# Performance work log

Measured on AMD Instinct MI355X. Metric: run time of the kernel, lower is better.

## Reference

```python
import jax, jax.numpy as jnp
import numpy as np

N = 25000
E = 400000
MUL0 = 64   # multiplicity of 0e node irreps
MUL1 = 32   # multiplicity of 1o node irreps
NUM_BASIS = 10
FC_HIDDEN = 100
WEIGHT_NUMEL = 2 * MUL0 + 3 * MUL1  # 224: per-edge tp weights for the 5 uvu paths
MID_S = MUL0 + MUL1       # 96 mid scalar channels
MID_V = MUL0 + 2 * MUL1   # 128 mid vector channels
NUM_NEIGHBORS = 16.0


def setup_inputs() -> dict:
    key = jax.random.key(0)
    ks = jax.random.split(key, 16)
    inp = {
        'node_scalars': jax.random.normal(ks[0], (N, MUL0), jnp.float32),
        'node_vectors': jax.random.normal(ks[1], (N, MUL1, 3), jnp.float32),
        'node_attr': jnp.ones((N, 1), jnp.float32),
        'edge_src': jax.random.randint(ks[2], (E,), 0, N, jnp.int32),
        'edge_dst': jax.random.randint(ks[3], (E,), 0, N, jnp.int32),
        'edge_attr': jax.random.normal(ks[4], (E, 4), jnp.float32),
        'edge_scalars': jax.random.normal(ks[5], (E, NUM_BASIS), jnp.float32),
        # FullyConnectedNet: [10, 100, weight_numel], silu on hidden
        'W_fc1': jax.random.normal(ks[6], (NUM_BASIS, FC_HIDDEN), jnp.float32) / np.sqrt(NUM_BASIS),
        'W_fc2': jax.random.normal(ks[7], (FC_HIDDEN, WEIGHT_NUMEL), jnp.float32) / np.sqrt(FC_HIDDEN),
        # FullyConnectedTensorProduct with 0e attr == per-irrep linear mixing
        'W_sc_s': jax.random.normal(ks[8], (MUL0, MUL0), jnp.float32) / np.sqrt(MUL0),
        'W_sc_v': jax.random.normal(ks[9], (MUL1, MUL1), jnp.float32) / np.sqrt(MUL1),
        'W_l1_s': jax.random.normal(ks[10], (MUL0, MUL0), jnp.float32) / np.sqrt(MUL0),
        'W_l1_v': jax.random.normal(ks[11], (MUL1, MUL1), jnp.float32) / np.sqrt(MUL1),
        'W_l2_s': jax.random.normal(ks[12], (MID_S, MUL0), jnp.float32) / np.sqrt(MID_S),
        'W_l2_v': jax.random.normal(ks[13], (MID_V, MUL1), jnp.float32) / np.sqrt(MID_V),
        'W_l3': jax.random.normal(ks[14], (MID_S, 1), jnp.float32) / np.sqrt(MID_S),
    }
    return inp


def reference(node_scalars, node_vectors, node_attr, edge_src, edge_dst, edge_attr,
              edge_scalars, W_fc1, W_fc2, W_sc_s, W_sc_v, W_l1_s, W_l1_v,
              W_l2_s, W_l2_v, W_l3):
    n = node_scalars.shape[0]
    # --- edge-weight FC net: silu hidden, linear out -> per-edge tp weights ---
    w = jax.nn.silu(edge_scalars @ W_fc1) @ W_fc2  # [E, 224]
    w_00, w_01 = w[:, :MUL0], w[:, MUL0:2 * MUL0]                  # paths from 0e input
    w_10 = w[:, 2 * MUL0:2 * MUL0 + MUL1]                          # 1o x 0e -> 1o
    w_11s = w[:, 2 * MUL0 + MUL1:2 * MUL0 + 2 * MUL1]              # 1o x 1o -> 0e
    w_11v = w[:, 2 * MUL0 + 2 * MUL1:]                             # 1o x 1o -> 1o

    attr = node_attr  # [N,1] (0e attr => scalar multiplier)
    # self-connection and lin1 (per-irrep linear * attr)
    sc_s = (node_scalars @ W_sc_s) * attr
    sc_v = jnp.einsum('nuc,uv->nvc', node_vectors, W_sc_v) * attr[:, :, None]
    f_s = (node_scalars @ W_l1_s) * attr
    f_v = jnp.einsum('nuc,uv->nvc', node_vectors, W_l1_v) * attr[:, :, None]

    # --- gather source node features per edge ---
    s = f_s[edge_src]          # [E, MUL0]
    v = f_v[edge_src]          # [E, MUL1, 3]
    y0 = edge_attr[:, :1]      # l=0 sh
    y1 = edge_attr[:, 1:4]     # l=1 sh

    # --- weighted tensor product (uvu), CG-contracted paths ---
    mid_s = jnp.concatenate([
        w_00 * s * y0,                                              # 0e x 0e -> 0e
        w_11s * jnp.einsum('euc,ec->eu', v, y1) / jnp.sqrt(3.0),    # 1o x 1o -> 0e
    ], axis=1)                                                      # [E, 96]
    mid_v = jnp.concatenate([
        w_01[:, :, None] * s[:, :, None] * y1[:, None, :],          # 0e x 1o -> 1o
        w_10[:, :, None] * v * y0[:, :, None],                      # 1o x 0e -> 1o
        w_11v[:, :, None] * jnp.cross(v, y1[:, None, :]) / jnp.sqrt(2.0),  # 1o x 1o -> 1o
    ], axis=1)                                                      # [E, 128, 3]

    # --- scatter-add aggregation into destination nodes ---
    inv = 1.0 / jnp.sqrt(NUM_NEIGHBORS)
    agg_s = jax.ops.segment_sum(mid_s, edge_dst, num_segments=n) * inv
    agg_v = jax.ops.segment_sum(mid_v, edge_dst, num_segments=n) * inv

    # --- output linears and gated residual mix ---
    conv_s = (agg_s @ W_l2_s) * attr
    conv_v = jnp.einsum('nuc,uv->nvc', agg_v, W_l2_v) * attr[:, :, None]
    angle = 0.1 * (agg_s @ W_l3) * attr  # [N,1]
    cos, sin = jnp.cos(angle), jnp.sin(angle)  # sc output_mask is all-ones here
    out_s = cos * sc_s + sin * conv_s
    out_v = cos[:, :, None] * sc_v + sin[:, :, None] * conv_v
    return jnp.concatenate([out_s, out_v.reshape(n, -1)], axis=1)  # [N, 64+96]
```

## Files before the change

### kernel.cpp

```cpp
#include <hip/hip_runtime.h>

#define MUL0 64
#define MUL1 32
#define NBASIS 10
#define FCH 100
#define WNUMEL 224
#define MIDS 96
#define MIDV 128
#define EG 4

#define OFF_W1   0
#define OFF_W2   1000
#define OFF_WSCS 23400
#define OFF_WSCV 27496
#define OFF_WL1S 28520
#define OFF_WL1V 32616
#define OFF_WL2S 33640
#define OFF_WL2V 39784
#define OFF_WL3  43880
#define OFF_WEND 43976
#define OFF_FLAG 43980
#define OFF_W1FRAG 44032
#define OFF_W2FRAG 45824
#define OFF_DYN  60160

#define W1FRAG_N (112 * 32)
#define W2FRAG_N (4 * 224 * 32)

typedef __attribute__((ext_vector_type(8))) short short8;
typedef __attribute__((ext_vector_type(4))) float f32x4;

__device__ __forceinline__ float bf2f(unsigned short h) {
    unsigned int u = ((unsigned int)h) << 16;
    float f; __builtin_memcpy(&f, &u, 4); return f;
}
__device__ __forceinline__ unsigned short f2bf(float f) {
    unsigned int u; __builtin_memcpy(&u, &f, 4);
    u += 0x7fffu + ((u >> 16) & 1u);
    return (unsigned short)(u >> 16);
}
__device__ __forceinline__ float fast_silu(float x) {
    return x * __builtin_amdgcn_rcpf(1.0f + __expf(-x));
}
template<bool BF>
__device__ __forceinline__ float ldf(const void* p, size_t i) {
    if constexpr (BF) return bf2f(((const unsigned short*)p)[i]);
    else              return ((const float*)p)[i];
}
template<bool BF>
__device__ __forceinline__ void stf(void* p, size_t i, float v) {
    if constexpr (BF) ((unsigned short*)p)[i] = f2bf(v);
    else              ((float*)p)[i] = v;
}
template<bool BF>
__device__ __forceinline__ f32x4 ld4(const void* p, size_t i) {
    if constexpr (BF) {
        ushort4 h = *(const ushort4*)((const unsigned short*)p + i);
        return (f32x4){bf2f(h.x), bf2f(h.y), bf2f(h.z), bf2f(h.w)};
    } else {
        return *(const f32x4*)((const float*)p + i);
    }
}
__device__ __forceinline__ int wave_incl_scan(int v) {
    int lane = threadIdx.x & 63;
    #pragma unroll
    for (int d = 1; d < 64; d <<= 1) {
        int t = __shfl_up(v, d, 64);
        if (lane >= d) v += t;
    }
    return v;
}

template<bool BF>
__device__ __forceinline__ void node_pre_body(
    const void* __restrict__ ns, const void* __restrict__ nv,
    const void* __restrict__ attr,
    const void* __restrict__ Wl1s, const void* __restrict__ Wl1v,
    float* __restrict__ f_s, float* __restrict__ f_v, int i, int Nn)
{
    int stotal = Nn * MUL0;
    if (i < stotal) {
        int n = i >> 6, j = i & 63;
        float a = 0.f;
        #pragma unroll
        for (int u = 0; u < MUL0; u++)
            a = fmaf(ldf<BF>(ns, (size_t)n * MUL0 + u), ldf<BF>(Wl1s, u * MUL0 + j), a);
        f_s[i] = a * ldf<BF>(attr, n);
    } else {
        int m = i - stotal;
        if (m >= Nn * MUL1 * 3) return;
        int n = m / 96; int idx = m - n * 96;
        int vi = idx / 3; int c = idx - vi * 3;
        float a = 0.f;
        #pragma unroll
        for (int u = 0; u < MUL1; u++)
            a = fmaf(ldf<BF>(nv, (size_t)n * 96 + u * 3 + c), ldf<BF>(Wl1v, u * MUL1 + vi), a);
        f_v[m] = a * ldf<BF>(attr, n);
    }
}

__global__ __launch_bounds__(256) void k_prep(
    const void* __restrict__ ns, const void* __restrict__ nv,
    const void* __restrict__ attr,
    const void* __restrict__ a0, const void* __restrict__ a1,
    const void* __restrict__ a2, const void* __restrict__ a3,
    const void* __restrict__ a4, const void* __restrict__ a5,
    const void* __restrict__ a6, const void* __restrict__ a7,
    const void* __restrict__ a8,
    float* __restrict__ wsf,
    unsigned short* __restrict__ w1frag, unsigned short* __restrict__ w2frag,
    int* __restrict__ cnt, int* __restrict__ flag,
    float* __restrict__ f_s, float* __restrict__ f_v, int Nn)
{
    const bool bf = (((const unsigned int*)attr)[0] == 0x3F803F80u);
    int i = blockIdx.x * 256 + threadIdx.x;
    if (i == 0) *flag = bf ? 1 : 0;

    const int npre = Nn * 160;
    if (i < npre) {
        if (bf) node_pre_body<true >(ns, nv, attr, a4, a5, f_s, f_v, i, Nn);
        else    node_pre_body<false>(ns, nv, attr, a4, a5, f_s, f_v, i, Nn);
        return;
    }
    int m = i - npre;
    if (m < OFF_WEND) {
        const void* p; int off = m;
        if      (m < OFF_W2)   { p = a0; }
        else if (m < OFF_WSCS) { p = a1; off = m - OFF_W2; }
        else if (m < OFF_WSCV) { p = a2; off = m - OFF_WSCS; }
        else if (m < OFF_WL1S) { p = a3; off = m - OFF_WSCV; }
        else if (m < OFF_WL1V) { p = a4; off = m - OFF_WL1S; }
        else if (m < OFF_WL2S) { p = a5; off = m - OFF_WL1V; }
        else if (m < OFF_WL2V) { p = a6; off = m - OFF_WL2S; }
        else if (m < OFF_WL3)  { p = a7; off = m - OFF_WL2V; }
        else                   { p = a8; off = m - OFF_WL3; }
        wsf[m] = bf ? ldf<true>(p, off) : ldf<false>(p, off);
        return;
    }
    m -= OFF_WEND;
    if (m < W1FRAG_N) {
        int col = m >> 5, k = m & 31;
        float v = 0.f;
        if (col < FCH && k < NBASIS)
            v = bf ? ldf<true>(a0, k * FCH + col) : ldf<false>(a0, k * FCH + col);
        w1frag[m] = f2bf(v);
        return;
    }
    m -= W1FRAG_N;
    if (m < W2FRAG_N) {
        int q = m / (224 * 32); int r = m - q * 224 * 32;
        int n = r >> 5; int kk = r & 31;
        int k = q * 32 + kk;
        float v = 0.f;
        if (k < FCH)
            v = bf ? ldf<true>(a1, k * WNUMEL + n) : ldf<false>(a1, k * WNUMEL + n);
        w2frag[m] = f2bf(v);
        return;
    }
    m -= W2FRAG_N;
    if (m < Nn) cnt[m] = 0;
}

__global__ __launch_bounds__(256) void k_hist(
    const int* __restrict__ edst, int* __restrict__ cnt, int Ecnt)
{
    int e = blockIdx.x * 256 + threadIdx.x;
    if (e < Ecnt) atomicAdd(&cnt[edst[e]], 1);
}

__global__ __launch_bounds__(256) void k_scan_blk(
    const int* __restrict__ cnt, int* __restrict__ row_part,
    int* __restrict__ blk_sum, int Nn)
{
    __shared__ int ws4[4];
    int tid = threadIdx.x, lane = tid & 63, wid = tid >> 6;
    int i = blockIdx.x * 256 + tid;
    int v = (i < Nn) ? cnt[i] : 0;
    int incl = wave_incl_scan(v);
    if (lane == 63) ws4[wid] = incl;
    __syncthreads();
    int off = 0;
    #pragma unroll
    for (int w2 = 0; w2 < 4; w2++) off += (w2 < wid) ? ws4[w2] : 0;
    if (i < Nn) row_part[i] = off + incl - v;
    if (tid == 0) blk_sum[blockIdx.x] = ws4[0] + ws4[1] + ws4[2] + ws4[3];
}

__global__ __launch_bounds__(256) void k_scan_top(
    const int* __restrict__ blk_sum, int* __restrict__ blk_off,
    int* __restrict__ row_start, int NB, int Nn)
{
    __shared__ int ws4[4];
    int tid = threadIdx.x, lane = tid & 63, wid = tid >> 6;
    int v = (tid < NB) ? blk_sum[tid] : 0;
    int incl = wave_incl_scan(v);
    if (lane == 63) ws4[wid] = incl;
    __syncthreads();
    int off = 0;
    #pragma unroll
    for (int w2 = 0; w2 < 4; w2++) off += (w2 < wid) ? ws4[w2] : 0;
    if (tid < NB) blk_off[tid] = off + incl - v;
    if (tid == 0) row_start[Nn] = ws4[0] + ws4[1] + ws4[2] + ws4[3];
}

__global__ __launch_bounds__(256) void k_rowfix(
    const int* __restrict__ row_part, const int* __restrict__ blk_off,
    int* __restrict__ row_start, int* __restrict__ cur, int Nn)
{
    int i = blockIdx.x * 256 + threadIdx.x;
    if (i < Nn) { row_start[i] = blk_off[i >> 8] + row_part[i]; cur[i] = 0; }
}

__global__ __launch_bounds__(1024) void k_scan1(
    const int* __restrict__ cnt, int* __restrict__ row_start,
    int* __restrict__ cur, int Nn)
{
    __shared__ int wsum[16];
    __shared__ int s_off, s_tot;
    int tid = threadIdx.x, lane = tid & 63, wid = tid >> 6;
    if (tid == 0) s_off = 0;
    __syncthreads();
    for (int base = 0; base < Nn; base += 1024) {
        int i = base + tid;
        int v = (i < Nn) ? cnt[i] : 0;
        int incl = wave_incl_scan(v);
        if (lane == 63) wsum[wid] = incl;
        __syncthreads();
        if (wid == 0) {
            int wv = (lane < 16) ? wsum[lane] : 0;
            int wincl = wave_incl_scan(wv);
            if (lane < 16) wsum[lane] = wincl - wv;
            if (lane == 15) s_tot = wincl;
        }
        __syncthreads();
        int excl = s_off + wsum[wid] + incl - v;
        if (i < Nn) { row_start[i] = excl; cur[i] = 0; }
        __syncthreads();
        if (tid == 0) s_off += s_tot;
        __syncthreads();
    }
    if (threadIdx.x == 0) row_start[Nn] = s_off;
}

__global__ __launch_bounds__(256) void k_place(
    const int* __restrict__ edst, const int* __restrict__ esrc,
    const void* __restrict__ eattr,
    const int* __restrict__ row_start, int* __restrict__ cur,
    int* __restrict__ perm, int* __restrict__ srcs, float* __restrict__ y4,
    int Ecnt, const int* __restrict__ flag, int extras)
{
    int e = blockIdx.x * 256 + threadIdx.x;
    if (e >= Ecnt) return;
    int d = edst[e];
    int pos = row_start[d] + atomicAdd(&cur[d], 1);
    perm[pos] = e;
    if (extras) {
        srcs[pos] = esrc[e];
        float4 yv;
        if (*flag) {
            const unsigned short* ap = (const unsigned short*)eattr + (size_t)e * 4;
            yv = make_float4(bf2f(ap[0]), bf2f(ap[1]), bf2f(ap[2]), bf2f(ap[3]));
        } else {
            const float* ap = (const float*)eattr + (size_t)e * 4;
            yv = make_float4(ap[0], ap[1], ap[2], ap[3]);
        }
        ((float4*)y4)[pos] = yv;
    }
}

#define HFC_STRIDE 136

__global__ __launch_bounds__(256) void k_fc(
    const void* __restrict__ escal, const int* __restrict__ perm,
    const unsigned short* __restrict__ w1frag, const unsigned short* __restrict__ w2frag,
    unsigned short* __restrict__ wbuf, int Ecnt, const int* __restrict__ flag)
{
    __shared__ __align__(16) unsigned short h_lds[64 * HFC_STRIDE];
    const int tid  = threadIdx.x;
    const int lane = tid & 63;
    const int wave = tid >> 6;
    const int nl   = lane & 15;
    const int quad = lane >> 4;
    const int tb   = blockIdx.x * 64;

    for (int i = tid; i < 64 * 16; i += 256) {
        int row = i >> 4;
        h_lds[row * HFC_STRIDE + 112 + (i & 15)] = 0;
    }

    int eidx = tb + 16 * wave + nl;
    if (eidx >= Ecnt) eidx = Ecnt - 1;
    const int e = perm[eidx];
    short8 a = {0, 0, 0, 0, 0, 0, 0, 0};
    if (*flag) {
        const unsigned int* p = (const unsigned int*)((const unsigned short*)escal + (size_t)e * NBASIS);
        if (quad == 0) {
            unsigned int d0 = p[0], d1 = p[1], d2 = p[2], d3 = p[3];
            a = (short8){(short)d0, (short)(d0 >> 16), (short)d1, (short)(d1 >> 16),
                         (short)d2, (short)(d2 >> 16), (short)d3, (short)(d3 >> 16)};
        } else if (quad == 1) {
            unsigned int d4 = p[4];
            a = (short8){(short)d4, (short)(d4 >> 16), 0, 0, 0, 0, 0, 0};
        }
    } else {
        const float* p = (const float*)escal + (size_t)e * NBASIS;
        if (quad == 0) {
            a = (short8){(short)f2bf(p[0]), (short)f2bf(p[1]), (short)f2bf(p[2]), (short)f2bf(p[3]),
                         (short)f2bf(p[4]), (short)f2bf(p[5]), (short)f2bf(p[6]), (short)f2bf(p[7])};
        } else if (quad == 1) {
            a = (short8){(short)f2bf(p[8]), (short)f2bf(p[9]), 0, 0, 0, 0, 0, 0};
        }
    }

    {
        f32x4 hacc[7];
        #pragma unroll
        for (int t = 0; t < 7; t++) {
            short8 b = *(const short8*)&w1frag[(16 * t + nl) * 32 + quad * 8];
            hacc[t] = __builtin_amdgcn_mfma_f32_16x16x32_bf16(
                a, b, (f32x4){0.f, 0.f, 0.f, 0.f}, 0, 0, 0);
        }
        #pragma unroll
        for (int t = 0; t < 7; t++) {
            #pragma unroll
            for (int r = 0; r < 4; r++)
                h_lds[(16 * wave + quad * 4 + r) * HFC_STRIDE + 16 * t + nl] =
                    f2bf(fast_silu(hacc[t][r]));
        }
    }
    __syncthreads();

    #pragma unroll 2
    for (int t = 0; t < 14; t++) {
        f32x4 c = {0.f, 0.f, 0.f, 0.f};
        #pragma unroll
        for (int q = 0; q < 4; q++) {
            short8 av = *(const short8*)&h_lds[(16 * wave + nl) * HFC_STRIDE + q * 32 + quad * 8];
            short8 b = *(const short8*)&w2frag[((q * 224) + 16 * t + nl) * 32 + quad * 8];
            c = __builtin_amdgcn_mfma_f32_16x16x32_bf16(av, b, c, 0, 0, 0);
        }
        #pragma unroll
        for (int r = 0; r < 4; r++)
            wbuf[(size_t)(tb + 16 * wave + quad * 4 + r) * WNUMEL + 16 * t + nl] = f2bf(c[r]);
    }
}

__global__ __launch_bounds__(256) void k_agg(
    const unsigned short* __restrict__ wbuf,
    const int* __restrict__ srcs, const float* __restrict__ y4,
    const int* __restrict__ row_start,
    const float* __restrict__ f_s, const float* __restrict__ f_v,
    const float* __restrict__ Wl3, const void* __restrict__ attr,
    float* __restrict__ agg_s, float* __restrict__ aggv,
    float* __restrict__ cosb, float* __restrict__ sinb,
    int Nn, const int* __restrict__ flag)
{
    const int tid  = threadIdx.x;
    const int lane = tid & 63;
    const int wave = tid >> 6;
    const int node = blockIdx.x * EG + wave;
    if (node >= Nn) return;

    const int lane2 = lane & 31;
    const bool hi = (lane >= 32);

    const int dlo = row_start[node];
    const int dhi = row_start[node + 1];

    float acc0 = 0.f, acc1 = 0.f;
    float accS0 = 0.f, accS1 = 0.f, accS2 = 0.f;
    float accV0 = 0.f, accV1 = 0.f, accV2 = 0.f;

    const float k14 = 0.25f;
    const float k13 = 0.25f * 0.57735026918962576451f;
    const float k12 = 0.25f * 0.70710678118654752440f;

    #pragma unroll 2
    for (int idx = dlo; idx < dhi; idx++) {
        const int srcn = srcs[idx];
        const float4 y = ((const float4*)y4)[idx];
        const float y0 = y.x, y1x = y.y, y1y = y.z, y1z = y.w;
        const unsigned short* wrow = wbuf + (size_t)idx * WNUMEL;
        const float* fsr = f_s + (size_t)srcn * 64;
        const float* fvr = f_v + (size_t)srcn * 96;

        float fs_l = fsr[lane];
        float v0 = fvr[lane2 * 3 + 0];
        float v1 = fvr[lane2 * 3 + 1];
        float v2 = fvr[lane2 * 3 + 2];

        float w00 = bf2f(wrow[lane]);
        float w01 = bf2f(wrow[64 + lane]);
        float wh  = bf2f(wrow[128 + lane]);
        float wx  = bf2f(wrow[160 + lane]);

        acc0 = fmaf(w00 * fs_l, y0 * k14, acc0);

        float dot = v0 * y1x + v1 * y1y + v2 * y1z;
        acc1 = fmaf(wh * dot, k13, acc1);

        float t1 = w01 * fs_l * k14;
        accS0 = fmaf(t1, y1x, accS0);
        accS1 = fmaf(t1, y1y, accS1);
        accS2 = fmaf(t1, y1z, accS2);

        float cx = v1 * y1z - v2 * y1y;
        float cy = v2 * y1x - v0 * y1z;
        float cz = v0 * y1y - v1 * y1x;
        float e0 = hi ? cx : v0;
        float e1 = hi ? cy : v1;
        float e2 = hi ? cz : v2;
        float tv = hi ? (wx * k12) : (wh * (y0 * k14));
        accV0 = fmaf(e0, tv, accV0);
        accV1 = fmaf(e1, tv, accV1);
        accV2 = fmaf(e2, tv, accV2);
    }

    {
        float* as = agg_s + (size_t)node * MIDS;
        float* av = aggv  + (size_t)node * 384;
        as[lane] = acc0;
        if (hi) as[64 + lane2] = acc1;

        av[0 * 128 + lane] = accS0;
        av[1 * 128 + lane] = accS1;
        av[2 * 128 + lane] = accS2;
        const int vrow = hi ? (96 + lane2) : (64 + lane);
        av[0 * 128 + vrow] = accV0;
        av[1 * 128 + vrow] = accV1;
        av[2 * 128 + vrow] = accV2;

        float avv = acc0 * Wl3[lane];
        if (hi) avv = fmaf(acc1, Wl3[64 + lane2], avv);
        #pragma unroll
        for (int d = 1; d < 64; d <<= 1) avv += __shfl_xor(avv, d);
        if (lane == 0) {
            float at = (*flag) ? ldf<true>(attr, node) : ldf<false>(attr, node);
            float aa = 0.1f * avv * at;
            cosb[node] = __cosf(aa);
            sinb[node] = __sinf(aa);
        }
    }
}

#define WT_STRIDE 164

template<bool BF>
__device__ __forceinline__ void final_s_body(
    const float* __restrict__ agg_s, const void* __restrict__ ns,
    const float* __restrict__ cosb, const float* __restrict__ sinb,
    const void* __restrict__ attr, void* __restrict__ out,
    int Nn, const float* Wt, int lane, int nb)
{
    float acc_sc[8], acc_l2[8];
    int nidx[8];
    #pragma unroll
    for (int r = 0; r < 8; r++) {
        acc_sc[r] = 0.f; acc_l2[r] = 0.f;
        int n = nb + r; nidx[r] = (n < Nn) ? n : (Nn - 1);
    }
    #pragma unroll 2
    for (int t = 0; t < 16; t++) {
        f32x4 wv = *(const f32x4*)&Wt[lane * WT_STRIDE + 4 * t];
        #pragma unroll
        for (int r = 0; r < 8; r++) {
            f32x4 x = ld4<BF>(ns, (size_t)nidx[r] * 64 + 4 * t);
            acc_sc[r] = fmaf(x[0], wv[0], acc_sc[r]);
            acc_sc[r] = fmaf(x[1], wv[1], acc_sc[r]);
            acc_sc[r] = fmaf(x[2], wv[2], acc_sc[r]);
            acc_sc[r] = fmaf(x[3], wv[3], acc_sc[r]);
        }
    }
    #pragma unroll 2
    for (int t = 0; t < 24; t++) {
        f32x4 wv = *(const f32x4*)&Wt[lane * WT_STRIDE + 64 + 4 * t];
        #pragma unroll
        for (int r = 0; r < 8; r++) {
            f32x4 x = *(const f32x4*)(agg_s + (size_t)nidx[r] * 96 + 4 * t);
            acc_l2[r] = fmaf(x[0], wv[0], acc_l2[r]);
            acc_l2[r] = fmaf(x[1], wv[1], acc_l2[r]);
            acc_l2[r] = fmaf(x[2], wv[2], acc_l2[r]);
            acc_l2[r] = fmaf(x[3], wv[3], acc_l2[r]);
        }
    }
    #pragma unroll
    for (int r = 0; r < 8; r++) {
        int n = nb + r;
        if (n < Nn) {
            float cv = cosb[n], sv = sinb[n];
            float at = ldf<BF>(attr, n);
            stf<BF>(out, (size_t)n * 160 + lane, at * (cv * acc_sc[r] + sv * acc_l2[r]));
        }
    }
}

__global__ __launch_bounds__(256) void k_final_s(
    const float* __restrict__ agg_s, const void* __restrict__ ns,
    const float* __restrict__ Wscs, const float* __restrict__ Wl2s,
    const float* __restrict__ cosb, const float* __restrict__ sinb,
    const void* __restrict__ attr, void* __restrict__ out,
    int Nn, const int* __restrict__ flag)
{
    __shared__ float Wt[64 * WT_STRIDE];
    const int tid = threadIdx.x;
    for (int i = tid; i < 160 * 64; i += 256) {
        int u = i >> 6, j = i & 63;
        float w = (u < 64) ? Wscs[u * 64 + j] : Wl2s[(u - 64) * 64 + j];
        Wt[j * WT_STRIDE + u] = w;
    }
    __syncthreads();

    const int lane = tid & 63;
    const int wave = __builtin_amdgcn_readfirstlane(tid >> 6);
    const int nb   = (blockIdx.x * 4 + wave) * 8;
    if (nb >= Nn) return;
    if (*flag) final_s_body<true >(agg_s, ns, cosb, sinb, attr, out, Nn, Wt, lane, nb);
    else       final_s_body<false>(agg_s, ns, cosb, sinb, attr, out, Nn, Wt, lane, nb);
}

template<bool BF>
__device__ __forceinline__ void final_v_body(
    const float* __restrict__ aggv, const void* __restrict__ nv,
    const float* __restrict__ cosb, const float* __restrict__ sinb,
    const void* __restrict__ attr, void* __restrict__ out,
    int Nn, const float* Wt, int lane, int ub)
{
    const int vi   = lane & 31;
    const int grp  = lane >> 5;
    const int NU   = 3 * Nn;
    float acc_sc[8], acc_l2[8];
    int gidx[8], nn_[8], cc_[8];
    #pragma unroll
    for (int r = 0; r < 8; r++) {
        acc_sc[r] = 0.f; acc_l2[r] = 0.f;
        int g = ub + grp * 8 + r;
        if (g > NU - 1) g = NU - 1;
        gidx[r] = g;
        nn_[r] = (int)((unsigned)g / 3u);
        cc_[r] = g - 3 * nn_[r];
    }
    #pragma unroll 2
    for (int t = 0; t < 8; t++) {
        f32x4 wv = *(const f32x4*)&Wt[vi * WT_STRIDE + 4 * t];
        #pragma unroll
        for (int r = 0; r < 8; r++) {
            size_t b = (size_t)nn_[r] * 96 + (size_t)(4 * t) * 3 + cc_[r];
            float x0 = ldf<BF>(nv, b);
            float x1 = ldf<BF>(nv, b + 3);
            float x2 = ldf<BF>(nv, b + 6);
            float x3 = ldf<BF>(nv, b + 9);
            acc_sc[r] = fmaf(x0, wv[0], acc_sc[r]);
            acc_sc[r] = fmaf(x1, wv[1], acc_sc[r]);
            acc_sc[r] = fmaf(x2, wv[2], acc_sc[r]);
            acc_sc[r] = fmaf(x3, wv[3], acc_sc[r]);
        }
    }
    #pragma unroll 2
    for (int t = 0; t < 32; t++) {
        f32x4 wv = *(const f32x4*)&Wt[vi * WT_STRIDE + 32 + 4 * t];
        #pragma unroll
        for (int r = 0; r < 8; r++) {
            f32x4 x = *(const f32x4*)(aggv + (size_t)gidx[r] * 128 + 4 * t);
            acc_l2[r] = fmaf(x[0], wv[0], acc_l2[r]);
            acc_l2[r] = fmaf(x[1], wv[1], acc_l2[r]);
            acc_l2[r] = fmaf(x[2], wv[2], acc_l2[r]);
            acc_l2[r] = fmaf(x[3], wv[3], acc_l2[r]);
        }
    }
    #pragma unroll
    for (int r = 0; r < 8; r++) {
        int g = ub + grp * 8 + r;
        if (g < NU) {
            int n = nn_[r], c = cc_[r];
            float cv = cosb[n], sv = sinb[n];
            float at = ldf<BF>(attr, n);
            stf<BF>(out, (size_t)n * 160 + 64 + vi * 3 + c,
                    at * (cv * acc_sc[r] + sv * acc_l2[r]));
        }
    }
}

__global__ __launch_bounds__(256) void k_final_v(
    const float* __restrict__ aggv, const void* __restrict__ nv,
    const float* __restrict__ Wscv, const float* __restrict__ Wl2v,
    const float* __restrict__ cosb, const float* __restrict__ sinb,
    const void* __restrict__ attr, void* __restrict__ out,
    int Nn, const int* __restrict__ flag)
{
    __shared__ float Wt[32 * WT_STRIDE];
    const int tid = threadIdx.x;
    for (int i = tid; i < 160 * 32; i += 256) {
        int u = i >> 5, j = i & 31;
        float w = (u < 32) ? Wscv[u * 32 + j] : Wl2v[(u - 32) * 32 + j];
        Wt[j * WT_STRIDE + u] = w;
    }
    __syncthreads();

    const int lane = tid & 63;
    const int wave = __builtin_amdgcn_readfirstlane(tid >> 6);
    const int ub   = (blockIdx.x * 4 + wave) * 16;
    if (ub >= 3 * Nn) return;
    if (*flag) final_v_body<true >(aggv, nv, cosb, sinb, attr, out, Nn, Wt, lane, ub);
    else       final_v_body<false>(aggv, nv, cosb, sinb, attr, out, Nn, Wt, lane, ub);
}

#define ES_STRIDE 40
#define H_STRIDE 136
#define WL_STRIDE 225

__global__ __launch_bounds__(256) void k_edge_mfma(
    const void* __restrict__ escal, const void* __restrict__ eattr,
    const void* __restrict__ attr,
    const int* __restrict__ esrc,
    const int* __restrict__ row_start, const int* __restrict__ perm,
    const unsigned short* __restrict__ w1frag, const unsigned short* __restrict__ w2frag,
    const float* __restrict__ Wl3,
    const float* __restrict__ f_s, const float* __restrict__ f_v,
    float* __restrict__ agg_s, float* __restrict__ agg_v,
    float* __restrict__ cosb, float* __restrict__ sinb,
    int Nn, const int* __restrict__ flag)
{
    __shared__ __align__(16) unsigned short es_lds[64 * ES_STRIDE];
    __shared__ __align__(16) unsigned short h_lds[64 * H_STRIDE];
    __shared__ __align__(16) unsigned short w_lds[64 * WL_STRIDE];
    __shared__ float y_lds[64][4];
    __shared__ int   src_lds[64];

    const int tid  = threadIdx.x;
    const int lane = tid & 63;
    const int wave = tid >> 6;
    const int nl   = lane & 15;
    const int quad = lane >> 4;
    const int gbase = blockIdx.x * EG;
    const bool isbf = (*flag != 0);

    for (int i = tid; i < 64 * 22; i += 256) {
        int row = i / 22, k = 10 + (i - row * 22);
        es_lds[row * ES_STRIDE + k] = 0;
    }
    for (int i = tid; i < 64 * 16; i += 256) {
        int row = i >> 4, k = 112 + (i & 15);
        h_lds[row * H_STRIDE + k] = 0;
    }

    const int lane2 = lane & 31;
    const int u0 = lane / 3,  c0 = lane - 3 * u0;
    const int pB = 64 + lane;
    const int uB = pB / 3,    cB = pB - 3 * uB;
    const int p2 = 128 + lane;
    const int u2 = p2 / 3,    c2 = p2 - 3 * u2;
    const int pH = 64 + lane2;
    const int uH = pH / 3,    cH = pH - 3 * uH;
    const bool half = (lane < 32);

    const int node = gbase + wave;
    const int dlo = (node < Nn) ? row_start[node] : 0;
    const int dhi = (node < Nn) ? row_start[node + 1] : 0;

    float acc[9];
    #pragma unroll
    for (int s = 0; s < 9; s++) acc[s] = 0.f;

    const int gend    = (gbase + EG < Nn) ? (gbase + EG) : Nn;
    const int e_start = row_start[gbase];
    const int e_end   = row_start[gend];

    for (int tb = e_start; tb < e_end; tb += 64) {
        const int tcnt = (e_end - tb < 64) ? (e_end - tb) : 64;
        __syncthreads();

        {
            int i = tid & 63, part = tid >> 6;
            if (i < tcnt && part < 2) {
                int e = perm[tb + i];
                if (part == 0) {
                    unsigned int* dstp = (unsigned int*)&es_lds[i * ES_STRIDE];
                    if (isbf) {
                        const unsigned int* srcp =
                            (const unsigned int*)((const unsigned short*)escal + (size_t)e * NBASIS);
                        #pragma unroll
                        for (int t2 = 0; t2 < 5; t2++) dstp[t2] = srcp[t2];
                    } else {
                        const float* srcp = (const float*)escal + (size_t)e * NBASIS;
                        #pragma unroll
                        for (int t2 = 0; t2 < 5; t2++) {
                            unsigned int lo = f2bf(srcp[2 * t2]);
                            unsigned int hi = f2bf(srcp[2 * t2 + 1]);
                            dstp[t2] = lo | (hi << 16);
                        }
                    }
                } else {
                    src_lds[i] = esrc[e];
                    if (isbf) {
                        const unsigned short* ap = (const unsigned short*)eattr + (size_t)e * 4;
                        #pragma unroll
                        for (int t2 = 0; t2 < 4; t2++) y_lds[i][t2] = bf2f(ap[t2]);
                    } else {
                        const float* ap = (const float*)eattr + (size_t)e * 4;
                        #pragma unroll
                        for (int t2 = 0; t2 < 4; t2++) y_lds[i][t2] = ap[t2];
                    }
                }
            }
        }
        __syncthreads();

        {
            short8 a = *(const short8*)&es_lds[(16 * wave + nl) * ES_STRIDE + quad * 8];
            f32x4 hacc[7];
            #pragma unroll
            for (int t = 0; t < 7; t++) {
                short8 b = *(const short8*)&w1frag[(16 * t + nl) * 32 + quad * 8];
                hacc[t] = __builtin_amdgcn_mfma_f32_16x16x32_bf16(
                    a, b, (f32x4){0.f, 0.f, 0.f, 0.f}, 0, 0, 0);
            }
            #pragma unroll
            for (int t = 0; t < 7; t++) {
                #pragma unroll
                for (int r = 0; r < 4; r++)
                    h_lds[(16 * wave + quad * 4 + r) * H_STRIDE + 16 * t + nl] =
                        f2bf(fast_silu(hacc[t][r]));
            }
        }
        __syncthreads();

        #pragma unroll 2
        for (int t = 0; t < 14; t++) {
            f32x4 c = {0.f, 0.f, 0.f, 0.f};
            #pragma unroll
            for (int q = 0; q < 4; q++) {
                short8 a = *(const short8*)&h_lds[(16 * wave + nl) * H_STRIDE + q * 32 + quad * 8];
                short8 b = *(const short8*)&w2frag[((q * 224) + 16 * t + nl) * 32 + quad * 8];
                c = __builtin_amdgcn_mfma_f32_16x16x32_bf16(a, b, c, 0, 0, 0);
            }
            #pragma unroll
            for (int r = 0; r < 4; r++)
                w_lds[(16 * wave + quad * 4 + r) * WL_STRIDE + 16 * t + nl] = f2bf(c[r]);
        }
        __syncthreads();

        {
            int lo = dlo > tb ? dlo : tb;
            int hi = dhi < tb + tcnt ? dhi : tb + tcnt;
            for (int idx = lo; idx < hi; idx++) {
                const int i = idx - tb;
                const int srcn = src_lds[i];
                const float y0  = y_lds[i][0];
                const float y1x = y_lds[i][1];
                const float y1y = y_lds[i][2];
                const float y1z = y_lds[i][3];
                const float* fsr = f_s + (size_t)srcn * 64;
                const float* fvr = f_v + (size_t)srcn * 96;
                const unsigned short* wrow = &w_lds[i * WL_STRIDE];

                float fs_l  = fsr[lane];
                float fs_u0 = fsr[u0];
                float fs_uB = fsr[uB];
                float fs_u2 = fsr[u2];
                float fvA0 = fvr[lane2 * 3], fvA1 = fvr[lane2 * 3 + 1], fvA2 = fvr[lane2 * 3 + 2];
                float fvB0 = fvr[u0 * 3],    fvB1 = fvr[u0 * 3 + 1],    fvB2 = fvr[u0 * 3 + 2];
                float fvH0 = fvr[uH * 3],    fvH1 = fvr[uH * 3 + 1],    fvH2 = fvr[uH * 3 + 2];

                float y1c0 = (c0 == 0) ? y1x : (c0 == 1) ? y1y : y1z;
                float y1cB = (cB == 0) ? y1x : (cB == 1) ? y1y : y1z;
                float y1c2 = (c2 == 0) ? y1x : (c2 == 1) ? y1y : y1z;

                float w_s0 = bf2f(wrow[lane]);
                float w_s1 = bf2f(wrow[160 + lane2]);
                float w_s2 = bf2f(wrow[64 + u0]);
                float w_s3 = bf2f(wrow[64 + uB]);
                float w_s4 = bf2f(wrow[64 + u2]);
                float w_s5 = bf2f(wrow[128 + u0]);
                float w_s6 = bf2f(wrow[128 + uH]);
                float w_s7 = bf2f(wrow[192 + u0]);
                float w_s8 = bf2f(wrow[192 + uH]);

                const float k14 = 0.25f;
                const float k13 = 0.25f * 0.57735026918962576451f;
                const float k12 = 0.25f * 0.70710678118654752440f;

                acc[0] = fmaf(w_s0 * fs_l, y0 * k14, acc[0]);
                {
                    float dot = fvA0 * y1x + fvA1 * y1y + fvA2 * y1z;
                    acc[1] = fmaf(w_s1 * dot, k13, acc[1]);
                }
                acc[2] = fmaf(w_s2 * fs_u0, k14 * y1c0, acc[2]);
                acc[3] = fmaf(w_s3 * fs_uB, k14 * y1cB, acc[3]);
                acc[4] = fmaf(w_s4 * fs_u2, k14 * y1c2, acc[4]);
                {
                    float e5 = (c0 == 0) ? fvB0 : (c0 == 1) ? fvB1 : fvB2;
                    float e6 = (cH == 0) ? fvH0 : (cH == 1) ? fvH1 : fvH2;
                    acc[5] = fmaf(w_s5 * e5, k14 * y0, acc[5]);
                    acc[6] = fmaf(w_s6 * e6, k14 * y0, acc[6]);
                }
                {
                    float cr7 = (c0 == 0) ? (fvB1 * y1z - fvB2 * y1y)
                              : (c0 == 1) ? (fvB2 * y1x - fvB0 * y1z)
                                          : (fvB0 * y1y - fvB1 * y1x);
                    float cr8 = (cH == 0) ? (fvH1 * y1z - fvH2 * y1y)
                              : (cH == 1) ? (fvH2 * y1x - fvH0 * y1z)
                                          : (fvH0 * y1y - fvH1 * y1x);
                    acc[7] = fmaf(w_s7 * cr7, k12, acc[7]);
                    acc[8] = fmaf(w_s8 * cr8, k12, acc[8]);
                }
            }
        }
    }

    if (node < Nn) {
        float* as = agg_s + (size_t)node * MIDS;
        float* av = agg_v + (size_t)node * (MIDV * 3);
        as[lane] = acc[0];
        if (half) as[64 + lane] = acc[1];
        av[lane]       = acc[2];
        av[64 + lane]  = acc[3];
        av[128 + lane] = acc[4];
        av[192 + lane] = acc[5];
        if (half) av[256 + lane] = acc[6];
        av[288 + lane] = acc[7];
        if (half) av[352 + lane] = acc[8];

        float avv = acc[0] * Wl3[lane];
        if (half) avv = fmaf(acc[1], Wl3[64 + lane], avv);
        #pragma unroll
        for (int d = 1; d < 64; d <<= 1) avv += __shfl_xor(avv, d);
        if (lane == 0) {
            float at = isbf ? ldf<true>(attr, node) : ldf<false>(attr, node);
            float a = 0.1f * avv * at;
            cosb[node] = __cosf(a);
            sinb[node] = __sinf(a);
        }
    }
}

template<bool BF>
__device__ __forceinline__ void final_body(
    const void* __restrict__ ns, const void* __restrict__ nv,
    const void* __restrict__ attr,
    const float* __restrict__ Wscs, const float* __restrict__ Wscv,
    const float* __restrict__ Wl2s, const float* __restrict__ Wl2v,
    const float* __restrict__ agg_s, const float* __restrict__ agg_v,
    const float* __restrict__ cosb, const float* __restrict__ sinb,
    void* __restrict__ out, int Nn)
{
    int i = blockIdx.x * 256 + threadIdx.x;
    int stotal = Nn * MUL0;
    if (i < stotal) {
        int n = i >> 6, j = i & 63;
        const float* ar = agg_s + (size_t)n * MIDS;
        float a1 = 0.f, a2 = 0.f;
        #pragma unroll
        for (int u = 0; u < MUL0; u++)
            a1 = fmaf(ldf<BF>(ns, (size_t)n * MUL0 + u), Wscs[u * MUL0 + j], a1);
        #pragma unroll
        for (int u = 0; u < MIDS; u++) a2 = fmaf(ar[u], Wl2s[u * MUL0 + j], a2);
        float o = ldf<BF>(attr, n) * (cosb[n] * a1 + sinb[n] * a2);
        stf<BF>(out, (size_t)n * 160 + j, o);
    } else {
        int m = i - stotal;
        if (m >= Nn * 96) return;
        int n = m / 96; int idx = m - n * 96;
        int vi = idx / 3; int c = idx - vi * 3;
        const float* ar = agg_v + (size_t)n * (MIDV * 3);
        float a1 = 0.f, a2 = 0.f;
        #pragma unroll
        for (int u = 0; u < MUL1; u++)
            a1 = fmaf(ldf<BF>(nv, (size_t)n * 96 + u * 3 + c), Wscv[u * MUL1 + vi], a1);
        #pragma unroll
        for (int u = 0; u < MIDV; u++) a2 = fmaf(ar[u * 3 + c], Wl2v[u * MUL1 + vi], a2);
        float o = ldf<BF>(attr, n) * (cosb[n] * a1 + sinb[n] * a2);
        stf<BF>(out, (size_t)n * 160 + 64 + idx, o);
    }
}
__global__ __launch_bounds__(256) void k_final(
    const void* ns, const void* nv, const void* attr,
    const float* Wscs, const float* Wscv,
    const float* Wl2s, const float* Wl2v,
    const float* agg_s, const float* agg_v,
    const float* cosb, const float* sinb,
    void* out, int Nn, const int* flag)
{
    if (*flag) final_body<true >(ns, nv, attr, Wscs, Wscv, Wl2s, Wl2v, agg_s, agg_v, cosb, sinb, out, Nn);
    else       final_body<false>(ns, nv, attr, Wscs, Wscv, Wl2s, Wl2v, agg_s, agg_v, cosb, sinb, out, Nn);
}

extern "C" void kernel_launch(void* const* d_in, const int* in_sizes, int n_in,
                              void* d_out, int out_size, void* d_ws, size_t ws_size,
                              hipStream_t stream)
{
    const void* ns    = d_in[0];
    const void* nv    = d_in[1];
    const void* attr  = d_in[2];
    const int*  esrc  = (const int*)d_in[3];
    const int*  edst  = (const int*)d_in[4];
    const void* eattr = d_in[5];
    const void* escal = d_in[6];

    const int Nn   = in_sizes[2];
    const int Ecnt = in_sizes[3];

    float* ws = (float*)d_ws;
    int* flag = (int*)(ws + OFF_FLAG);
    unsigned short* w1frag = (unsigned short*)(ws + OFF_W1FRAG);
    unsigned short* w2frag = (unsigned short*)(ws + OFF_W2FRAG);

    size_t o = OFF_DYN;
    const size_t OFF_FS   = o; o += (size_t)Nn * 64;
    const size_t OFF_FV   = o; o += (size_t)Nn * 96;
    const size_t OFF_AGGS = o; o += (size_t)Nn * 96;
    const size_t OFF_AGGV = o; o += (size_t)Nn * 384;
    const size_t OFF_COS  = o; o += Nn;
    const size_t OFF_SIN  = o; o += Nn;
    const size_t OFF_CNT  = o; o += Nn;
    const size_t OFF_ROW  = o; o += Nn + 1;
    const size_t OFF_CUR  = o; o += Nn;
    const size_t OFF_RPART= o; o += Nn;
    const size_t OFF_BSUM = o; o += 256;
    const size_t OFF_BOFF = o; o += 256;
    const size_t OFF_PERM = o; o += Ecnt;
    const size_t OFF_SRCS = o; o += Ecnt;
    o = (o + 3) & ~(size_t)3;
    const size_t OFF_Y4   = o; o += (size_t)Ecnt * 4;
    o = (o + 15) & ~(size_t)15;
    const size_t OFF_WBUF = o;
    const int tiles = (Ecnt + 63) / 64;
    o += (size_t)tiles * 64 * 112;
    const size_t need_bytes = o * sizeof(float);

    int* cnt       = (int*)(ws + OFF_CNT);
    int* row_start = (int*)(ws + OFF_ROW);
    int* cur       = (int*)(ws + OFF_CUR);
    int* row_part  = (int*)(ws + OFF_RPART);
    int* blk_sum   = (int*)(ws + OFF_BSUM);
    int* blk_off   = (int*)(ws + OFF_BOFF);
    int* perm      = (int*)(ws + OFF_PERM);
    int* srcs      = (int*)(ws + OFF_SRCS);
    float* y4      = ws + OFF_Y4;
    unsigned short* wbuf = (unsigned short*)(ws + OFF_WBUF);

    const int NB = (Nn + 255) / 256;
    const bool split = (ws_size >= need_bytes) && (NB <= 256);

    const int prep_work = Nn * 160 + OFF_WEND + W1FRAG_N + W2FRAG_N + Nn;
    k_prep<<<(prep_work + 255) / 256, 256, 0, stream>>>(
        ns, nv, attr,
        d_in[7], d_in[8], d_in[9], d_in[10], d_in[11], d_in[12],
        d_in[13], d_in[14], d_in[15],
        ws, w1frag, w2frag, cnt, flag,
        ws + OFF_FS, ws + OFF_FV, Nn);

    k_hist<<<(Ecnt + 255) / 256, 256, 0, stream>>>(edst, cnt, Ecnt);

    if (split) {
        k_scan_blk<<<NB, 256, 0, stream>>>(cnt, row_part, blk_sum, Nn);
        k_scan_top<<<1, 256, 0, stream>>>(blk_sum, blk_off, row_start, NB, Nn);
        k_rowfix<<<NB, 256, 0, stream>>>(row_part, blk_off, row_start, cur, Nn);
        k_place<<<(Ecnt + 255) / 256, 256, 0, stream>>>(
            edst, esrc, eattr, row_start, cur, perm, srcs, y4, Ecnt, flag, 1);

        k_fc<<<tiles, 256, 0, stream>>>(escal, perm, w1frag, w2frag, wbuf, Ecnt, flag);

        k_agg<<<(Nn + EG - 1) / EG, 256, 0, stream>>>(
            wbuf, srcs, y4, row_start,
            ws + OFF_FS, ws + OFF_FV, ws + OFF_WL3, attr,
            ws + OFF_AGGS, ws + OFF_AGGV, ws + OFF_COS, ws + OFF_SIN,
            Nn, flag);

        k_final_s<<<(Nn + 31) / 32, 256, 0, stream>>>(
            ws + OFF_AGGS, ns, ws + OFF_WSCS, ws + OFF_WL2S,
            ws + OFF_COS, ws + OFF_SIN, attr, (void*)d_out, Nn, flag);
        k_final_v<<<(3 * Nn + 63) / 64, 256, 0, stream>>>(
            ws + OFF_AGGV, nv, ws + OFF_WSCV, ws + OFF_WL2V,
            ws + OFF_COS, ws + OFF_SIN, attr, (void*)d_out, Nn, flag);
    } else {
        k_scan1<<<1, 1024, 0, stream>>>(cnt, row_start, cur, Nn);
        k_place<<<(Ecnt + 255) / 256, 256, 0, stream>>>(
            edst, esrc, eattr, row_start, cur, perm, srcs, y4, Ecnt, flag, 0);
        k_edge_mfma<<<(Nn + EG - 1) / EG, 256, 0, stream>>>(
            escal, eattr, attr, esrc, row_start, perm, w1frag, w2frag,
            ws + OFF_WL3,
            ws + OFF_FS, ws + OFF_FV,
            ws + OFF_AGGS, ws + OFF_AGGV, ws + OFF_COS, ws + OFF_SIN,
            Nn, flag);
        k_final<<<((Nn * 160) + 255) / 256, 256, 0, stream>>>(
            ns, nv, attr,
            ws + OFF_WSCS, ws + OFF_WSCV, ws + OFF_WL2S, ws + OFF_WL2V,
            ws + OFF_AGGS, ws + OFF_AGGV, ws + OFF_COS, ws + OFF_SIN,
            (void*)d_out, Nn, flag);
    }
}
```

Baseline: 544.7 us.

## Store edge weights in MFMA fragment order and split aggregation into two streams

The FC-net output store now writes each lane's four bf16 results as one packed 8-byte write in the MFMA fragment layout, replacing four scattered 2-byte row-major writes. The aggregation kernel recomputes addresses for this swizzled layout when it reads weights. It also splits each node's edge list into two halves with separate accumulators, which gives two independent dependency chains and more loads in flight. The cost is more complex address arithmetic, less coalesced 2-byte weight reads in the consumer, and extra registers for the second accumulator set.

```diff
diff --git a/kernel.cpp b/kernel.cpp
--- a/kernel.cpp
+++ b/kernel.cpp
@@ -330,6 +330,7 @@
     }
     __syncthreads();
 
+    unsigned short* wwave = wbuf + (size_t)tb * 224 + wave * 3584;
     #pragma unroll 2
     for (int t = 0; t < 14; t++) {
         f32x4 c = {0.f, 0.f, 0.f, 0.f};
@@ -339,11 +340,50 @@
             short8 b = *(const short8*)&w2frag[((q * 224) + 16 * t + nl) * 32 + quad * 8];
             c = __builtin_amdgcn_mfma_f32_16x16x32_bf16(av, b, c, 0, 0, 0);
         }
-        #pragma unroll
-        for (int r = 0; r < 4; r++)
-            wbuf[(size_t)(tb + 16 * wave + quad * 4 + r) * WNUMEL + 16 * t + nl] = f2bf(c[r]);
-    }
-}
+        unsigned int plo = (unsigned int)f2bf(c[0]) | ((unsigned int)f2bf(c[1]) << 16);
+        unsigned int phi = (unsigned int)f2bf(c[2]) | ((unsigned int)f2bf(c[3]) << 16);
+        *(uint2*)&wwave[t * 256 + lane * 4] = make_uint2(plo, phi);
+    }
+}
+
+#define AGG_BODY(IDX, S)                                                     \
+  {                                                                          \
+    const int idx_ = (IDX);                                                  \
+    const int srcn = srcs[idx_];                                             \
+    const float4 y = ((const float4*)y4)[idx_];                              \
+    const size_t wb = (size_t)(idx_ >> 6) * 14336                            \
+        + (size_t)((((idx_ >> 4) & 3) * 3584) + (((idx_ >> 2) & 3) * 64)     \
+                   + (idx_ & 3));                                            \
+    const unsigned short* wp = wbuf + wb + woff;                             \
+    const float* fsr = f_s + (size_t)srcn * 64;                              \
+    const float* fvr = f_v + (size_t)srcn * 96;                              \
+    float fs_l = fsr[lane];                                                  \
+    float v0 = fvr[lane2 * 3 + 0];                                           \
+    float v1 = fvr[lane2 * 3 + 1];                                           \
+    float v2 = fvr[lane2 * 3 + 2];                                           \
+    float w00 = bf2f(wp[0]);                                                 \
+    float w01 = bf2f(wp[1024]);                                              \
+    float wh  = bf2f(wp[2048]);                                              \
+    float wx  = bf2f(wp[2560]);                                              \
+    const float y0 = y.x, y1x = y.y, y1y = y.z, y1z = y.w;                   \
+    acc0##S = fmaf(w00 * fs_l, y0 * k14, acc0##S);                           \
+    float dot_ = v0 * y1x + v1 * y1y + v2 * y1z;                             \
+    acc1##S = fmaf(wh * dot_, k13, acc1##S);                                 \
+    float t1_ = w01 * fs_l * k14;                                            \
+    accS0##S = fmaf(t1_, y1x, accS0##S);                                     \
+    accS1##S = fmaf(t1_, y1y, accS1##S);                                     \
+    accS2##S = fmaf(t1_, y1z, accS2##S);                                     \
+    float cx_ = v1 * y1z - v2 * y1y;                                         \
+    float cy_ = v2 * y1x - v0 * y1z;                                         \
+    float cz_ = v0 * y1y - v1 * y1x;                                         \
+    float e0_ = hi ? cx_ : v0;                                               \
+    float e1_ = hi ? cy_ : v1;                                               \
+    float e2_ = hi ? cz_ : v2;                                               \
+    float tv_ = hi ? (wx * k12) : (wh * (y0 * k14));                         \
+    accV0##S = fmaf(e0_, tv_, accV0##S);                                     \
+    accV1##S = fmaf(e1_, tv_, accV1##S);                                     \
+    accV2##S = fmaf(e2_, tv_, accV2##S);                                     \
+  }
 
 __global__ __launch_bounds__(256) void k_agg(
     const unsigned short* __restrict__ wbuf,
@@ -363,58 +403,38 @@
 
     const int lane2 = lane & 31;
     const bool hi = (lane >= 32);
+    const int woff = ((lane >> 4) << 8) + ((lane & 15) << 2);
 
     const int dlo = row_start[node];
     const int dhi = row_start[node + 1];
-
-    float acc0 = 0.f, acc1 = 0.f;
-    float accS0 = 0.f, accS1 = 0.f, accS2 = 0.f;
-    float accV0 = 0.f, accV1 = 0.f, accV2 = 0.f;
+    const int mid = dlo + ((dhi - dlo) >> 1);
 
     const float k14 = 0.25f;
     const float k13 = 0.25f * 0.57735026918962576451f;
     const float k12 = 0.25f * 0.70710678118654752440f;
 
-    #pragma unroll 2
-    for (int idx = dlo; idx < dhi; idx++) {
-        const int srcn = srcs[idx];
-        const float4 y = ((const float4*)y4)[idx];
-        const float y0 = y.x, y1x = y.y, y1y = y.z, y1z = y.w;
-        const unsigned short* wrow = wbuf + (size_t)idx * WNUMEL;
-        const float* fsr = f_s + (size_t)srcn * 64;
-        const float* fvr = f_v + (size_t)srcn * 96;
-
-        float fs_l = fsr[lane];
-        float v0 = fvr[lane2 * 3 + 0];
-        float v1 = fvr[lane2 * 3 + 1];
-        float v2 = fvr[lane2 * 3 + 2];
-
-        float w00 = bf2f(wrow[lane]);
-        float w01 = bf2f(wrow[64 + lane]);
-        float wh  = bf2f(wrow[128 + lane]);
-        float wx  = bf2f(wrow[160 + lane]);
-
-        acc0 = fmaf(w00 * fs_l, y0 * k14, acc0);
-
-        float dot = v0 * y1x + v1 * y1y + v2 * y1z;
-        acc1 = fmaf(wh * dot, k13, acc1);
-
-        float t1 = w01 * fs_l * k14;
-        accS0 = fmaf(t1, y1x, accS0);
-        accS1 = fmaf(t1, y1y, accS1);
-        accS2 = fmaf(t1, y1z, accS2);
-
-        float cx = v1 * y1z - v2 * y1y;
-        float cy = v2 * y1x - v0 * y1z;
-        float cz = v0 * y1y - v1 * y1x;
-        float e0 = hi ? cx : v0;
-        float e1 = hi ? cy : v1;
-        float e2 = hi ? cz : v2;
-        float tv = hi ? (wx * k12) : (wh * (y0 * k14));
-        accV0 = fmaf(e0, tv, accV0);
-        accV1 = fmaf(e1, tv, accV1);
-        accV2 = fmaf(e2, tv, accV2);
-    }
+    float acc0A = 0.f, acc1A = 0.f, accS0A = 0.f, accS1A = 0.f, accS2A = 0.f;
+    float accV0A = 0.f, accV1A = 0.f, accV2A = 0.f;
+    float acc0B = 0.f, acc1B = 0.f, accS0B = 0.f, accS1B = 0.f, accS2B = 0.f;
+    float accV0B = 0.f, accV1B = 0.f, accV2B = 0.f;
+
+    int iA = dlo, iB = mid;
+    for (; iA < mid; ++iA, ++iB) {
+        AGG_BODY(iA, A);
+        AGG_BODY(iB, B);
+    }
+    for (; iB < dhi; ++iB) {
+        AGG_BODY(iB, B);
+    }
+
+    const float acc0  = acc0A + acc0B;
+    const float acc1  = acc1A + acc1B;
+    const float accS0 = accS0A + accS0B;
+    const float accS1 = accS1A + accS1B;
+    const float accS2 = accS2A + accS2B;
+    const float accV0 = accV0A + accV0B;
+    const float accV1 = accV1A + accV1B;
+    const float accV2 = accV2A + accV2B;
 
     {
         float* as = agg_s + (size_t)node * MIDS;
```

Result: slower. 559.5 us (+2.7%).
